# Optimization experiments

Measured on AMD Instinct MI355X. Metric: run time of the kernel, lower is better.

## Reference

```python
import jax, jax.numpy as jnp
import numpy as np

NUM_LEVELS = 4
RADIUS = 4


def _avg_pool2(x):
    # 2x2 stride-2 average pool over the last two dims of a 5D array, VALID padding
    s = jax.lax.reduce_window(x, 0.0, jax.lax.add, (1, 1, 1, 2, 2), (1, 1, 1, 2, 2), 'VALID')
    return s / 4.0


def _forward(fmap1, fmap2, coords):
    B, C, Hf, Wf = fmap1.shape
    _, N, _, H, W = coords.shape
    K = 2 * RADIUS + 1

    # all-pairs correlation: (B, H1, W1, H2, W2), scaled by 1/sqrt(C)
    f1 = fmap1.reshape(B, C, Hf * Wf)
    f2 = fmap2.reshape(B, C, Hf * Wf)
    corr = jnp.einsum('bcp,bcq->bpq', f1, f2) / jnp.sqrt(jnp.asarray(C, fmap1.dtype))
    corr = corr.reshape(B, Hf, Wf, Hf, Wf)

    pyramid = [corr]
    c = corr
    for _ in range(NUM_LEVELS - 1):
        c = _avg_pool2(c)
        pyramid.append(c)

    # coords channels: 0 = x, 1 = y  ->  (B, N, H, W, 2)
    cf = jnp.moveaxis(coords, 2, -1)

    d = jnp.linspace(-RADIUS, RADIUS, K, dtype=corr.dtype)
    # matches torch.stack(torch.meshgrid(dy, dx, indexing='ij'), axis=-1)
    delta = jnp.stack(jnp.meshgrid(d, d, indexing='ij'), axis=-1)  # (K, K, 2)

    bi = jnp.arange(B)[:, None, None, None, None]
    hi = jnp.arange(H)[None, None, :, None, None]
    wi = jnp.arange(W)[None, None, None, :, None]

    outs = []
    for i, cl in enumerate(pyramid):
        h2, w2 = cl.shape[-2], cl.shape[-1]
        # sampling coords (B, N, H, W, K, K, 2)
        sc = cf[..., None, None, :] / (2.0 ** i) + delta
        # grid_sample(align_corners=True) with coords pre-clamped to [-1,1]
        # == bilinear sample with pixel coords clamped to the valid range
        x = jnp.clip(sc[..., 0], 0.0, w2 - 1)
        y = jnp.clip(sc[..., 1], 0.0, h2 - 1)
        x0 = jnp.floor(x)
        y0 = jnp.floor(y)
        fx = (x - x0).reshape(B, N, H, W, K * K)
        fy = (y - y0).reshape(B, N, H, W, K * K)
        x0i = x0.astype(jnp.int32).reshape(B, N, H, W, K * K)
        y0i = y0.astype(jnp.int32).reshape(B, N, H, W, K * K)
        x1i = jnp.minimum(x0i + 1, w2 - 1)  # weight fx is 0 at the boundary
        y1i = jnp.minimum(y0i + 1, h2 - 1)

        cl_flat = cl.reshape(B, H, W, h2 * w2)  # query grid == feature grid (H==Hf, W==Wf)

        def gather(yi, xi):
            idx = yi * w2 + xi  # (B, N, H, W, K*K)
            return cl_flat[bi, hi, wi, idx]

        v = (gather(y0i, x0i) * (1 - fy) * (1 - fx)
             + gather(y0i, x1i) * (1 - fy) * fx
             + gather(y1i, x0i) * fy * (1 - fx)
             + gather(y1i, x1i) * fy * fx)
        outs.append(v)  # (B, N, H, W, K*K)

    out = jnp.concatenate(outs, axis=-1)  # (B, N, H, W, num_levels*K*K)
    # torch: (B,N,H,W,Cc).reshape(B, N*Cc, H, W) -- a raw row-major reshape
    out = out.reshape(B, N * out.shape[-1], H, W)
    return out.astype(jnp.float32)


def setup_inputs() -> dict:
    key = jax.random.key(0)
    k1, k2, k3 = jax.random.split(key, 3)
    B, C, H, W, N = 2, 256, 64, 64, 8
    fmap1 = jax.random.normal(k1, (B, C, H, W), dtype=jnp.float32)
    fmap2 = jax.random.normal(k2, (B, C, H, W), dtype=jnp.float32)
    coords = jax.random.uniform(k3, (B, N, 2, H, W), dtype=jnp.float32) * (W - 1)
    return {"fmap1": fmap1, "fmap2": fmap2, "coords": coords}


def reference(fmap1, fmap2, coords):
    return _forward(fmap1, fmap2, coords)
```

## Files before the change

kernel.cpp:

```cpp
#include <hip/hip_runtime.h>
#include <hip/hip_bf16.h>
#include <stdint.h>

#define B_   2
#define C_   256
#define P_   4096
#define N_   8
#define OUTC 2592

typedef __bf16 bf16x8 __attribute__((ext_vector_type(8)));
typedef float floatx4 __attribute__((ext_vector_type(4)));

__device__ __forceinline__ float bf2f(unsigned int u16) {
    union { unsigned int i; float f; } x; x.i = u16 << 16; return x.f;
}
__device__ __forceinline__ unsigned int f2bf(float f) {
    union { float f; unsigned int i; } x; x.f = f;
    unsigned int u = x.i + 0x7FFFu + ((x.i >> 16) & 1u);
    return u >> 16;
}

__global__ void conv_t(const float* __restrict__ in, __hip_bfloat16* __restrict__ out) {
    __shared__ float tile[32][33];
    int b  = blockIdx.z;
    int p0 = blockIdx.x * 32;
    int c0 = blockIdx.y * 32;
    int tx = threadIdx.x;
    int ty0 = threadIdx.y;
    const float* ip = in + ((size_t)b * C_ + c0) * P_ + p0;
    for (int r = 0; r < 4; r++) {
        int ty = ty0 + r * 8;
        tile[ty][tx] = ip[(size_t)ty * P_ + tx];
    }
    __syncthreads();
    __hip_bfloat16* op = out + ((size_t)b * P_ + p0) * C_ + c0;
    for (int r = 0; r < 4; r++) {
        int ty = ty0 + r * 8;
        op[(size_t)ty * C_ + tx] = __float2bfloat16(tile[tx][ty]);
    }
}

__global__ __launch_bounds__(256) void gemm_corr(const __hip_bfloat16* __restrict__ A,
                                                 const __hip_bfloat16* __restrict__ Bm,
                                                 unsigned short* __restrict__ Cmat) {
    __shared__ __align__(16) __hip_bfloat16 lA[128 * 32];
    __shared__ __align__(16) __hip_bfloat16 lB[128 * 32];
    const int b  = blockIdx.z;
    const int m0 = blockIdx.y * 128;
    const int n0 = blockIdx.x * 128;
    const __hip_bfloat16* Ab = A  + (size_t)b * P_ * C_;
    const __hip_bfloat16* Bb = Bm + (size_t)b * P_ * C_;
    unsigned short* Cb = Cmat + (size_t)b * P_ * P_;

    const int tid  = threadIdx.x;
    const int lane = tid & 63;
    const int w    = tid >> 6;
    const int wm   = w & 1, wn = w >> 1;

    floatx4 acc[4][4];
    for (int i = 0; i < 4; i++)
        for (int j = 0; j < 4; j++)
            acc[i][j] = floatx4{0.f, 0.f, 0.f, 0.f};

    const int srow = w * 16 + (lane >> 2);
    const int scol = (lane & 3) * 8;

    for (int k0 = 0; k0 < C_; k0 += 32) {
        for (int j = 0; j < 2; j++) {
            int row = j * 64 + srow;
            const __hip_bfloat16* ga = Ab + (size_t)(m0 + row) * C_ + k0 + scol;
            const __hip_bfloat16* gb = Bb + (size_t)(n0 + row) * C_ + k0 + scol;
            __hip_bfloat16* la = lA + (j * 64 + w * 16) * 32;
            __hip_bfloat16* lb = lB + (j * 64 + w * 16) * 32;
            __builtin_amdgcn_global_load_lds((const __attribute__((address_space(1))) void*)ga,
                                             (__attribute__((address_space(3))) void*)la, 16, 0, 0);
            __builtin_amdgcn_global_load_lds((const __attribute__((address_space(1))) void*)gb,
                                             (__attribute__((address_space(3))) void*)lb, 16, 0, 0);
        }
        __syncthreads();
        const int kq   = (lane >> 4) * 8;
        const int rsel = lane & 15;
        bf16x8 af[4], bfv[4];
        for (int i = 0; i < 4; i++) {
            af[i]  = *(const bf16x8*)&lA[(wm * 64 + i * 16 + rsel) * 32 + kq];
            bfv[i] = *(const bf16x8*)&lB[(wn * 64 + i * 16 + rsel) * 32 + kq];
        }
        for (int i = 0; i < 4; i++)
            for (int j = 0; j < 4; j++)
                acc[i][j] = __builtin_amdgcn_mfma_f32_16x16x32_bf16(af[i], bfv[j], acc[i][j], 0, 0, 0);
        __syncthreads();
    }

    const float scale = 0.0625f;
    const int colb  = n0 + wn * 64 + (lane & 15);
    const int rbase = m0 + wm * 64 + ((lane >> 4) * 4);
    for (int i = 0; i < 4; i++)
        for (int j = 0; j < 4; j++)
            for (int r = 0; r < 4; r++)
                Cb[(size_t)(rbase + i * 16 + r) * P_ + colb + j * 16] =
                    (unsigned short)f2bf(acc[i][j][r] * scale);
}

template<int WIN, int WOUT>
__global__ void pool2b(const unsigned int* __restrict__ in, unsigned int* __restrict__ out,
                       int npair) {
    int i = blockIdx.x * blockDim.x + threadIdx.x;
    if (i >= npair) return;
    int e = i * 2;
    int x = e & (WOUT - 1);
    int y = (e / WOUT) & (WOUT - 1);
    int s = e / (WOUT * WOUT);
    int rowu = ((s * WIN + 2 * y) * WIN) / 2 + x;
    unsigned int a0 = in[rowu],            a1 = in[rowu + 1];
    unsigned int b0 = in[rowu + WIN / 2],  b1 = in[rowu + WIN / 2 + 1];
    float s0 = 0.25f * (bf2f(a0 & 0xffff) + bf2f(a0 >> 16) + bf2f(b0 & 0xffff) + bf2f(b0 >> 16));
    float s1 = 0.25f * (bf2f(a1 & 0xffff) + bf2f(a1 >> 16) + bf2f(b1 & 0xffff) + bf2f(b1 >> 16));
    out[i] = f2bf(s0) | (f2bf(s1) << 16);
}

__global__ __launch_bounds__(256) void sample_k(const unsigned short* __restrict__ c0,
                                                const unsigned short* __restrict__ c1,
                                                const unsigned short* __restrict__ c2,
                                                const unsigned short* __restrict__ c3,
                                                const float* __restrict__ coords,
                                                float* __restrict__ outp) {
    __shared__ float sl[5560];
    __shared__ float cs[16];
    __shared__ unsigned int xtp[288];
    __shared__ float        xtf[288];
    __shared__ unsigned int ytp[288];
    __shared__ float        ytf[288];
    __shared__ unsigned int ctb[324];

    const int bp = blockIdx.x;
    const int b  = bp >> 12;
    const int p  = bp & 4095;
    const int tid = threadIdx.x;

    {
        const uint2* g0 = (const uint2*)(c0 + (size_t)bp * 4096);
        for (int i = tid; i < 1024; i += 256) {
            uint2 v = g0[i];
            int e = i * 4, x = e & 63, y = e >> 6;
            float* d = sl + y * 65 + x;
            d[0] = bf2f(v.x & 0xffff); d[1] = bf2f(v.x >> 16);
            d[2] = bf2f(v.y & 0xffff); d[3] = bf2f(v.y >> 16);
        }
        const uint2* g1 = (const uint2*)(c1 + (size_t)bp * 1024);
        {
            uint2 v = g1[tid];
            int e = tid * 4, x = e & 31, y = e >> 5;
            float* d = sl + 4160 + y * 33 + x;
            d[0] = bf2f(v.x & 0xffff); d[1] = bf2f(v.x >> 16);
            d[2] = bf2f(v.y & 0xffff); d[3] = bf2f(v.y >> 16);
        }
        if (tid < 64) {
            uint2 v = ((const uint2*)(c2 + (size_t)bp * 256))[tid];
            int e = tid * 4, x = e & 15, y = e >> 4;
            float* d = sl + 5216 + y * 17 + x;
            d[0] = bf2f(v.x & 0xffff); d[1] = bf2f(v.x >> 16);
            d[2] = bf2f(v.y & 0xffff); d[3] = bf2f(v.y >> 16);
        }
        if (tid < 16) {
            uint2 v = ((const uint2*)(c3 + (size_t)bp * 64))[tid];
            int e = tid * 4, x = e & 7, y = e >> 3;
            float* d = sl + 5488 + y * 9 + x;
            d[0] = bf2f(v.x & 0xffff); d[1] = bf2f(v.x >> 16);
            d[2] = bf2f(v.y & 0xffff); d[3] = bf2f(v.y >> 16);
        }
        if (tid < 16) cs[tid] = coords[(size_t)(b * 16 + tid) * 4096 + p];
    }
    __syncthreads();

    for (int t = tid; t < 324; t += 256) {
        if (t < 288) {
            int n = t / 36, rem = t - n * 36;
            int l = rem / 9, dd = rem - l * 9;
            int wl = 64 >> l;
            int pw = (l == 0) ? 65 : (l == 1) ? 33 : (l == 2) ? 17 : 9;
            float inv = 1.0f / (float)(1 << l);
            float mx = (float)(wl - 1);
            float cx = cs[n * 2 + 0], cy = cs[n * 2 + 1];
            float xx = fminf(fmaxf(cx * inv + (float)(dd - 4), 0.0f), mx);
            float yy = fminf(fmaxf(cy * inv + (float)(dd - 4), 0.0f), mx);
            float x0f = floorf(xx), y0f = floorf(yy);
            int x0 = (int)x0f, y0 = (int)y0f;
            int x1 = min(x0 + 1, wl - 1), y1 = min(y0 + 1, wl - 1);
            xtp[t] = ((unsigned int)x0 << 8) | (unsigned int)x1;
            xtf[t] = xx - x0f;
            ytp[t] = ((unsigned int)(y0 * pw) << 16) | (unsigned int)(y1 * pw);
            ytf[t] = yy - y0f;
        }
        int c = t;
        int l = c / 81, k = c - l * 81;
        int i9 = k / 9, j9 = k - i9 * 9;
        int off = (l == 0) ? 0 : (l == 1) ? 4160 : (l == 2) ? 5216 : 5488;
        ctb[c] = ((unsigned int)off << 16) | ((unsigned int)(l * 9 + i9) << 8)
               | (unsigned int)(l * 9 + j9);
    }
    __syncthreads();

    const size_t outbase = (size_t)b * ((size_t)N_ * P_ * 324) + (size_t)p * 324;
    for (int o = tid; o < OUTC; o += 256) {
        int n = o / 324;
        int c = o - n * 324;
        unsigned int cv = ctb[c];
        int off = cv >> 16;
        int tb  = n * 36;
        unsigned int xp = xtp[tb + ((cv >> 8) & 255)];
        float        fx = xtf[tb + ((cv >> 8) & 255)];
        unsigned int yp = ytp[tb + (cv & 255)];
        float        fy = ytf[tb + (cv & 255)];
        int x0 = xp >> 8, x1 = xp & 255;
        const float* r0 = sl + off + (yp >> 16);
        const float* r1 = sl + off + (yp & 0xffff);
        float v00 = r0[x0], v01 = r0[x1];
        float v10 = r1[x0], v11 = r1[x1];
        float vx0 = v00 + fx * (v01 - v00);
        float vx1 = v10 + fx * (v11 - v10);
        float v   = vx0 + fy * (vx1 - vx0);
        outp[outbase + (size_t)n * (324 * 4095) + o] = v;
    }
}

extern "C" void kernel_launch(void* const* d_in, const int* in_sizes, int n_in,
                              void* d_out, int out_size, void* d_ws, size_t ws_size,
                              hipStream_t stream) {
    const float* fmap1  = (const float*)d_in[0];
    const float* fmap2  = (const float*)d_in[1];
    const float* coords = (const float*)d_in[2];
    float* out = (float*)d_out;

    char* ws = (char*)d_ws;
    size_t off = 0;
    auto alloc = [&](size_t bytes) {
        void* ptr = ws + off;
        off += (bytes + 255) & ~(size_t)255;
        return ptr;
    };
    __hip_bfloat16* f1t = (__hip_bfloat16*)alloc((size_t)B_ * P_ * C_ * 2);
    __hip_bfloat16* f2t = (__hip_bfloat16*)alloc((size_t)B_ * P_ * C_ * 2);
    unsigned short* corr0 = (unsigned short*)alloc((size_t)B_ * P_ * 4096 * 2);
    unsigned short* corr1 = (unsigned short*)alloc((size_t)B_ * P_ * 1024 * 2);
    unsigned short* corr2 = (unsigned short*)alloc((size_t)B_ * P_ * 256 * 2);
    unsigned short* corr3 = (unsigned short*)alloc((size_t)B_ * P_ * 64 * 2);

    dim3 tb(32, 8);
    conv_t<<<dim3(128, 8, B_), tb, 0, stream>>>(fmap1, f1t);
    conv_t<<<dim3(128, 8, B_), tb, 0, stream>>>(fmap2, f2t);

    gemm_corr<<<dim3(32, 32, B_), dim3(256), 0, stream>>>(f1t, f2t, corr0);

    int np1 = B_ * P_ * 32 * 32 / 2;
    int np2 = B_ * P_ * 16 * 16 / 2;
    int np3 = B_ * P_ * 8 * 8 / 2;
    pool2b<64, 32><<<(np1 + 255) / 256, 256, 0, stream>>>((const unsigned int*)corr0,
                                                          (unsigned int*)corr1, np1);
    pool2b<32, 16><<<(np2 + 255) / 256, 256, 0, stream>>>((const unsigned int*)corr1,
                                                          (unsigned int*)corr2, np2);
    pool2b<16, 8><<<(np3 + 255) / 256, 256, 0, stream>>>((const unsigned int*)corr2,
                                                         (unsigned int*)corr3, np3);

    sample_k<<<B_ * P_, 256, 0, stream>>>(corr0, corr1, corr2, corr3, coords, out);
}
```

Baseline: 189.3 us.

## Fuse pyramid pooling, merge transposes, remap GEMM tiles, keep bf16 in LDS

The two transpose launches are merged into one, and the three pooling kernels become a single per-row pyramid kernel that builds every level in shared memory. This avoids re-reading the intermediate levels from global memory. The GEMM uses a 1D grid with a swizzled block order to improve L2 reuse. The sampling kernel keeps correlation values in LDS as bf16 with padded rows and packs its index tables into float2. This halves LDS footprint and staging work but adds bf16 conversions on each gather.

New measurement: 180.2 us. -4.9%, faster.

```diff
diff --git a/kernel.cpp b/kernel.cpp
--- a/kernel.cpp
+++ b/kernel.cpp
@@ -20,9 +20,13 @@
     return u >> 16;
 }
 
-__global__ void conv_t(const float* __restrict__ in, __hip_bfloat16* __restrict__ out) {
+__global__ void conv_both(const float* __restrict__ in1, const float* __restrict__ in2,
+                          __hip_bfloat16* __restrict__ out1, __hip_bfloat16* __restrict__ out2) {
     __shared__ float tile[32][33];
-    int b  = blockIdx.z;
+    int which = blockIdx.z >> 1;
+    int b  = blockIdx.z & 1;
+    const float* in = which ? in2 : in1;
+    __hip_bfloat16* out = which ? out2 : out1;
     int p0 = blockIdx.x * 32;
     int c0 = blockIdx.y * 32;
     int tx = threadIdx.x;
@@ -45,12 +49,17 @@
                                                  unsigned short* __restrict__ Cmat) {
     __shared__ __align__(16) __hip_bfloat16 lA[128 * 32];
     __shared__ __align__(16) __hip_bfloat16 lB[128 * 32];
-    const int b  = blockIdx.z;
-    const int m0 = blockIdx.y * 128;
-    const int n0 = blockIdx.x * 128;
-    const __hip_bfloat16* Ab = A  + (size_t)b * P_ * C_;
-    const __hip_bfloat16* Bb = Bm + (size_t)b * P_ * C_;
-    unsigned short* Cb = Cmat + (size_t)b * P_ * P_;
+    const int id = blockIdx.x;
+    const int bz = id >> 10;
+    const int r_ = id & 1023;
+    const int s_ = r_ >> 3;
+    const int by = (r_ & 7) * 4 + (s_ >> 5);
+    const int bx = s_ & 31;
+    const int m0 = by * 128;
+    const int n0 = bx * 128;
+    const __hip_bfloat16* Ab = A  + (size_t)bz * P_ * C_;
+    const __hip_bfloat16* Bb = Bm + (size_t)bz * P_ * C_;
+    unsigned short* Cb = Cmat + (size_t)bz * P_ * P_;
 
     const int tid  = threadIdx.x;
     const int lane = tid & 63;
@@ -101,21 +110,60 @@
                     (unsigned short)f2bf(acc[i][j][r] * scale);
 }
 
-template<int WIN, int WOUT>
-__global__ void pool2b(const unsigned int* __restrict__ in, unsigned int* __restrict__ out,
-                       int npair) {
-    int i = blockIdx.x * blockDim.x + threadIdx.x;
-    if (i >= npair) return;
-    int e = i * 2;
-    int x = e & (WOUT - 1);
-    int y = (e / WOUT) & (WOUT - 1);
-    int s = e / (WOUT * WOUT);
-    int rowu = ((s * WIN + 2 * y) * WIN) / 2 + x;
-    unsigned int a0 = in[rowu],            a1 = in[rowu + 1];
-    unsigned int b0 = in[rowu + WIN / 2],  b1 = in[rowu + WIN / 2 + 1];
-    float s0 = 0.25f * (bf2f(a0 & 0xffff) + bf2f(a0 >> 16) + bf2f(b0 & 0xffff) + bf2f(b0 >> 16));
-    float s1 = 0.25f * (bf2f(a1 & 0xffff) + bf2f(a1 >> 16) + bf2f(b1 & 0xffff) + bf2f(b1 >> 16));
-    out[i] = f2bf(s0) | (f2bf(s1) << 16);
+__global__ __launch_bounds__(256) void pyramid(const unsigned int* __restrict__ c0,
+                                               unsigned int* __restrict__ c1,
+                                               unsigned int* __restrict__ c2,
+                                               unsigned int* __restrict__ c3) {
+    __shared__ unsigned int L0[2048];
+    __shared__ unsigned int L1[512];
+    __shared__ unsigned int L2[128];
+    const int bp = blockIdx.x;
+    const int tid = threadIdx.x;
+    {
+        const uint2* g = (const uint2*)(c0 + (size_t)bp * 2048);
+        uint2* d = (uint2*)L0;
+        for (int i = tid; i < 1024; i += 256) d[i] = g[i];
+    }
+    __syncthreads();
+    for (int t = tid; t < 512; t += 256) {
+        int x = t & 15;
+        int y = t >> 4;
+        unsigned int a = L0[(2 * y) * 32 + 2 * x];
+        unsigned int a2 = L0[(2 * y) * 32 + 2 * x + 1];
+        unsigned int b = L0[(2 * y + 1) * 32 + 2 * x];
+        unsigned int b2 = L0[(2 * y + 1) * 32 + 2 * x + 1];
+        float s0 = 0.25f * (bf2f(a & 0xffff) + bf2f(a >> 16) + bf2f(b & 0xffff) + bf2f(b >> 16));
+        float s1 = 0.25f * (bf2f(a2 & 0xffff) + bf2f(a2 >> 16) + bf2f(b2 & 0xffff) + bf2f(b2 >> 16));
+        unsigned int u = f2bf(s0) | (f2bf(s1) << 16);
+        L1[t] = u;
+        c1[(size_t)bp * 512 + t] = u;
+    }
+    __syncthreads();
+    if (tid < 128) {
+        int x = tid & 7;
+        int y = tid >> 3;
+        unsigned int a = L1[(2 * y) * 16 + 2 * x];
+        unsigned int a2 = L1[(2 * y) * 16 + 2 * x + 1];
+        unsigned int b = L1[(2 * y + 1) * 16 + 2 * x];
+        unsigned int b2 = L1[(2 * y + 1) * 16 + 2 * x + 1];
+        float s0 = 0.25f * (bf2f(a & 0xffff) + bf2f(a >> 16) + bf2f(b & 0xffff) + bf2f(b >> 16));
+        float s1 = 0.25f * (bf2f(a2 & 0xffff) + bf2f(a2 >> 16) + bf2f(b2 & 0xffff) + bf2f(b2 >> 16));
+        unsigned int u = f2bf(s0) | (f2bf(s1) << 16);
+        L2[tid] = u;
+        c2[(size_t)bp * 128 + tid] = u;
+    }
+    __syncthreads();
+    if (tid < 32) {
+        int x = tid & 3;
+        int y = tid >> 2;
+        unsigned int a = L2[(2 * y) * 8 + 2 * x];
+        unsigned int a2 = L2[(2 * y) * 8 + 2 * x + 1];
+        unsigned int b = L2[(2 * y + 1) * 8 + 2 * x];
+        unsigned int b2 = L2[(2 * y + 1) * 8 + 2 * x + 1];
+        float s0 = 0.25f * (bf2f(a & 0xffff) + bf2f(a >> 16) + bf2f(b & 0xffff) + bf2f(b >> 16));
+        float s1 = 0.25f * (bf2f(a2 & 0xffff) + bf2f(a2 >> 16) + bf2f(b2 & 0xffff) + bf2f(b2 >> 16));
+        c3[(size_t)bp * 32 + tid] = f2bf(s0) | (f2bf(s1) << 16);
+    }
 }
 
 __global__ __launch_bounds__(256) void sample_k(const unsigned short* __restrict__ c0,
@@ -124,50 +172,36 @@
                                                 const unsigned short* __restrict__ c3,
                                                 const float* __restrict__ coords,
                                                 float* __restrict__ outp) {
-    __shared__ float sl[5560];
+    __shared__ unsigned short sl16[5680];
     __shared__ float cs[16];
-    __shared__ unsigned int xtp[288];
-    __shared__ float        xtf[288];
-    __shared__ unsigned int ytp[288];
-    __shared__ float        ytf[288];
+    __shared__ float2 xt[288];
+    __shared__ float2 yt[288];
     __shared__ unsigned int ctb[324];
 
     const int bp = blockIdx.x;
     const int b  = bp >> 12;
     const int p  = bp & 4095;
     const int tid = threadIdx.x;
+    unsigned int* slu = (unsigned int*)sl16;
 
     {
         const uint2* g0 = (const uint2*)(c0 + (size_t)bp * 4096);
         for (int i = tid; i < 1024; i += 256) {
             uint2 v = g0[i];
-            int e = i * 4, x = e & 63, y = e >> 6;
-            float* d = sl + y * 65 + x;
-            d[0] = bf2f(v.x & 0xffff); d[1] = bf2f(v.x >> 16);
-            d[2] = bf2f(v.y & 0xffff); d[3] = bf2f(v.y >> 16);
-        }
-        const uint2* g1 = (const uint2*)(c1 + (size_t)bp * 1024);
-        {
-            uint2 v = g1[tid];
-            int e = tid * 4, x = e & 31, y = e >> 5;
-            float* d = sl + 4160 + y * 33 + x;
-            d[0] = bf2f(v.x & 0xffff); d[1] = bf2f(v.x >> 16);
-            d[2] = bf2f(v.y & 0xffff); d[3] = bf2f(v.y >> 16);
-        }
-        if (tid < 64) {
-            uint2 v = ((const uint2*)(c2 + (size_t)bp * 256))[tid];
-            int e = tid * 4, x = e & 15, y = e >> 4;
-            float* d = sl + 5216 + y * 17 + x;
-            d[0] = bf2f(v.x & 0xffff); d[1] = bf2f(v.x >> 16);
-            d[2] = bf2f(v.y & 0xffff); d[3] = bf2f(v.y >> 16);
-        }
-        if (tid < 16) {
-            uint2 v = ((const uint2*)(c3 + (size_t)bp * 64))[tid];
-            int e = tid * 4, x = e & 7, y = e >> 3;
-            float* d = sl + 5488 + y * 9 + x;
-            d[0] = bf2f(v.x & 0xffff); d[1] = bf2f(v.x >> 16);
-            d[2] = bf2f(v.y & 0xffff); d[3] = bf2f(v.y >> 16);
-        }
+            int e = 4 * i;
+            int y = e >> 6, x = e & 63;
+            int u = (y * 66 + x) >> 1;
+            slu[u] = v.x; slu[u + 1] = v.y;
+        }
+        const unsigned int* g1 = (const unsigned int*)(c1 + (size_t)bp * 1024);
+        for (int i = tid; i < 512; i += 256)
+            slu[2112 + (i >> 4) * 17 + (i & 15)] = g1[i];
+        if (tid < 128)
+            slu[2656 + (tid >> 3) * 9 + (tid & 7)] =
+                ((const unsigned int*)(c2 + (size_t)bp * 256))[tid];
+        if (tid < 32)
+            slu[2800 + (tid >> 2) * 5 + (tid & 3)] =
+                ((const unsigned int*)(c3 + (size_t)bp * 64))[tid];
         if (tid < 16) cs[tid] = coords[(size_t)(b * 16 + tid) * 4096 + p];
     }
     __syncthreads();
@@ -177,7 +211,8 @@
             int n = t / 36, rem = t - n * 36;
             int l = rem / 9, dd = rem - l * 9;
             int wl = 64 >> l;
-            int pw = (l == 0) ? 65 : (l == 1) ? 33 : (l == 2) ? 17 : 9;
+            int pw   = (l == 0) ? 66 : (l == 1) ? 34 : (l == 2) ? 18 : 10;
+            int base = (l == 0) ? 0  : (l == 1) ? 4224 : (l == 2) ? 5312 : 5600;
             float inv = 1.0f / (float)(1 << l);
             float mx = (float)(wl - 1);
             float cx = cs[n * 2 + 0], cy = cs[n * 2 + 1];
@@ -186,17 +221,16 @@
             float x0f = floorf(xx), y0f = floorf(yy);
             int x0 = (int)x0f, y0 = (int)y0f;
             int x1 = min(x0 + 1, wl - 1), y1 = min(y0 + 1, wl - 1);
-            xtp[t] = ((unsigned int)x0 << 8) | (unsigned int)x1;
-            xtf[t] = xx - x0f;
-            ytp[t] = ((unsigned int)(y0 * pw) << 16) | (unsigned int)(y1 * pw);
-            ytf[t] = yy - y0f;
+            unsigned int xb = (unsigned int)x0 | ((unsigned int)x1 << 8);
+            unsigned int yb = (unsigned int)(base + y0 * pw)
+                            | ((unsigned int)(base + y1 * pw) << 16);
+            xt[t] = make_float2(xx - x0f, __uint_as_float(xb));
+            yt[t] = make_float2(yy - y0f, __uint_as_float(yb));
         }
         int c = t;
         int l = c / 81, k = c - l * 81;
         int i9 = k / 9, j9 = k - i9 * 9;
-        int off = (l == 0) ? 0 : (l == 1) ? 4160 : (l == 2) ? 5216 : 5488;
-        ctb[c] = ((unsigned int)off << 16) | ((unsigned int)(l * 9 + i9) << 8)
-               | (unsigned int)(l * 9 + j9);
+        ctb[c] = ((unsigned int)(l * 9 + i9) << 8) | (unsigned int)(l * 9 + j9);
     }
     __syncthreads();
 
@@ -205,17 +239,18 @@
         int n = o / 324;
         int c = o - n * 324;
         unsigned int cv = ctb[c];
-        int off = cv >> 16;
-        int tb  = n * 36;
-        unsigned int xp = xtp[tb + ((cv >> 8) & 255)];
-        float        fx = xtf[tb + ((cv >> 8) & 255)];
-        unsigned int yp = ytp[tb + (cv & 255)];
-        float        fy = ytf[tb + (cv & 255)];
-        int x0 = xp >> 8, x1 = xp & 255;
-        const float* r0 = sl + off + (yp >> 16);
-        const float* r1 = sl + off + (yp & 0xffff);
-        float v00 = r0[x0], v01 = r0[x1];
-        float v10 = r1[x0], v11 = r1[x1];
+        int tb = n * 36;
+        float2 xv = xt[tb + (cv >> 8)];
+        float2 yv = yt[tb + (cv & 255)];
+        unsigned int xb = __float_as_uint(xv.y);
+        unsigned int yb = __float_as_uint(yv.y);
+        int x0 = xb & 255, x1 = xb >> 8;
+        int r0 = yb & 0xffff, r1 = yb >> 16;
+        float fx = xv.x, fy = yv.x;
+        float v00 = bf2f(sl16[r0 + x0]);
+        float v01 = bf2f(sl16[r0 + x1]);
+        float v10 = bf2f(sl16[r1 + x0]);
+        float v11 = bf2f(sl16[r1 + x1]);
         float vx0 = v00 + fx * (v01 - v00);
         float vx1 = v10 + fx * (v11 - v10);
         float v   = vx0 + fy * (vx1 - vx0);
@@ -245,21 +280,14 @@
     unsigned short* corr2 = (unsigned short*)alloc((size_t)B_ * P_ * 256 * 2);
     unsigned short* corr3 = (unsigned short*)alloc((size_t)B_ * P_ * 64 * 2);
 
-    dim3 tb(32, 8);
-    conv_t<<<dim3(128, 8, B_), tb, 0, stream>>>(fmap1, f1t);
-    conv_t<<<dim3(128, 8, B_), tb, 0, stream>>>(fmap2, f2t);
-
-    gemm_corr<<<dim3(32, 32, B_), dim3(256), 0, stream>>>(f1t, f2t, corr0);
-
-    int np1 = B_ * P_ * 32 * 32 / 2;
-    int np2 = B_ * P_ * 16 * 16 / 2;
-    int np3 = B_ * P_ * 8 * 8 / 2;
-    pool2b<64, 32><<<(np1 + 255) / 256, 256, 0, stream>>>((const unsigned int*)corr0,
-                                                          (unsigned int*)corr1, np1);
-    pool2b<32, 16><<<(np2 + 255) / 256, 256, 0, stream>>>((const unsigned int*)corr1,
-                                                          (unsigned int*)corr2, np2);
-    pool2b<16, 8><<<(np3 + 255) / 256, 256, 0, stream>>>((const unsigned int*)corr2,
-                                                         (unsigned int*)corr3, np3);
-
-    sample_k<<<B_ * P_, 256, 0, stream>>>(corr0, corr1, corr2, corr3, coords, out);
-}
+    conv_both<<<dim3(128, 8, 2 * B_), dim3(32, 8), 0, stream>>>(fmap1, fmap2, f1t, f2t);
+
+    gemm_corr<<<dim3(2048), dim3(256), 0, stream>>>(f1t, f2t, corr0);
+
+    pyramid<<<dim3(B_ * P_), dim3(256), 0, stream>>>((const unsigned int*)corr0,
+                                                     (unsigned int*)corr1,
+                                                     (unsigned int*)corr2,
+                                                     (unsigned int*)corr3);
+
+    sample_k<<<dim3(B_ * P_), dim3(256), 0, stream>>>(corr0, corr1, corr2, corr3, coords, out);
+}
```
